# Kernel tuning notes

Hardware: AMD Instinct MI355X
Metric: run time of the kernel (lower is better)

## Reference

```python
import jax, jax.numpy as jnp
import numpy as np

N_NODES = 50000


def setup_inputs() -> dict:
    key = jax.random.key(0)
    k1, k2, k3, k4, k5 = jax.random.split(key, 5)
    N, E, D, U = N_NODES, 1600000, 128, 128
    node_features = jax.random.normal(k1, (N, D), dtype=jnp.float32)
    edge_src = jax.random.randint(k2, (E,), 0, N, dtype=jnp.int32)
    edge_dst = jax.random.randint(k3, (E,), 0, N, dtype=jnp.int32)
    edge_weight = jax.random.uniform(k4, (E,), dtype=jnp.float32)
    W = jax.random.normal(k5, (D, U), dtype=jnp.float32) * (1.0 / np.sqrt(D))
    b = jnp.zeros((U,), dtype=jnp.float32)
    return {"node_features": node_features, "edge_src": edge_src,
            "edge_dst": edge_dst, "edge_weight": edge_weight, "W": W, "b": b}


def reference(node_features, edge_src, edge_dst, edge_weight, W, b):
    # embedding_lookup_sparse_v2(..., combiner='mean'):
    #   agg[i] = sum_{e: src[e]=i} w[e] * feat[dst[e]] / sum_{e: src[e]=i} w[e]
    gathered = node_features[edge_dst] * edge_weight[:, None]        # [E, D]
    num = jax.ops.segment_sum(gathered, edge_src, num_segments=N_NODES)   # [N, D]
    den = jax.ops.segment_sum(edge_weight, edge_src, num_segments=N_NODES)  # [N]
    agg = num / jnp.maximum(den, 1e-12)[:, None]
    # Dense(units, activation='relu'); dropout is identity at inference
    return jax.nn.relu(agg @ W + b)
```

## Files before the change

kernel.cpp:

```cpp
#include <hip/hip_runtime.h>
#include <hip/hip_bf16.h>


typedef unsigned int vuint4 __attribute__((ext_vector_type(4)));
typedef short bf16x8 __attribute__((ext_vector_type(8)));
typedef float f32x4 __attribute__((ext_vector_type(4)));

#define SRCSH 8
#define BNODES 256
#define BCAP 9728
#define PCAP 11776
#define NBLK 512

__device__ __forceinline__ unsigned short f2bf(float f) {
    unsigned u = __float_as_uint(f);
    unsigned r = (u + 0x7fff + ((u >> 16) & 1)) >> 16;
    return (unsigned short)r;
}
__device__ __forceinline__ float bf2f(unsigned short h) {
    return __uint_as_float(((unsigned)h) << 16);
}

__global__ __launch_bounds__(256)
void histA_kernel(const float* __restrict__ feat, ushort* __restrict__ featb,
                  const float* __restrict__ W, ushort* __restrict__ WT,
                  const int* __restrict__ esrc, int* __restrict__ cnt,
                  int E, int nbuk, int N, int D) {
    __shared__ int hcnt[256];
    int tid = threadIdx.x, blk = blockIdx.x;

    {
        int gid = blk * 256 + tid;
        int gstr = NBLK * 256;
        int nf4 = N * D / 4;
        for (int i = gid; i < nf4; i += gstr) {
            float4 v = ((const float4*)feat)[i];
            ushort4 r;
            r.x = f2bf(v.x); r.y = f2bf(v.y); r.z = f2bf(v.z); r.w = f2bf(v.w);
            ((ushort4*)featb)[i] = r;
        }
        int nw = D * D;
        for (int i = gid; i < nw; i += gstr) {
            int u = i >> 7, k = i & 127;
            WT[i] = f2bf(W[k * 128 + u]);
        }
    }

    hcnt[tid] = 0;
    __syncthreads();

    int per = ((E + NBLK - 1) / NBLK + 3) & ~3;
    int lo = blk * per;
    int hi = lo + per; if (hi > E) hi = E;
    for (int i4 = (lo >> 2) + tid; i4 < (hi >> 2); i4 += 256) {
        int4 s = ((const int4*)esrc)[i4];
        atomicAdd(&hcnt[s.x >> SRCSH], 1);
        atomicAdd(&hcnt[s.y >> SRCSH], 1);
        atomicAdd(&hcnt[s.z >> SRCSH], 1);
        atomicAdd(&hcnt[s.w >> SRCSH], 1);
    }
    __syncthreads();
    if (tid < nbuk) cnt[blk * nbuk + tid] = hcnt[tid];
}

__global__ __launch_bounds__(256)
void scanB_kernel(const int* __restrict__ cnt, int* __restrict__ hbase,
                  int* __restrict__ gtot, int nbuk) {
    int lane = threadIdx.x & 63, wid = threadIdx.x >> 6;
    int b = blockIdx.x * 4 + wid;
    if (b >= nbuk) return;

    int v[8]; int run = 0;
    #pragma unroll
    for (int i = 0; i < 8; ++i) {
        v[i] = cnt[(lane * 8 + i) * nbuk + b];
        run += v[i];
    }
    int x = run;
    #pragma unroll
    for (int off = 1; off < 64; off <<= 1) {
        int y = __shfl_up(x, off, 64);
        if (lane >= off) x += y;
    }
    int excl = x - run;
    #pragma unroll
    for (int i = 0; i < 8; ++i) {
        hbase[b * NBLK + lane * 8 + i] = excl;
        excl += v[i];
    }
    if (lane == 63) gtot[b] = x;
}

__global__ __launch_bounds__(256)
void scatterC_kernel(const int* __restrict__ esrc, const int* __restrict__ edst,
                     const float* __restrict__ ew, const int* __restrict__ hbase,
                     unsigned long long* __restrict__ staging, int E, int nbuk) {
    __shared__ int hb[256];
    __shared__ int hoff[256];
    int tid = threadIdx.x, blk = blockIdx.x;
    if (tid < nbuk) { hb[tid] = hbase[tid * NBLK + blk]; }
    hoff[tid] = 0;
    __syncthreads();

    int per = ((E + NBLK - 1) / NBLK + 3) & ~3;
    int lo = blk * per;
    int hi = lo + per; if (hi > E) hi = E;
    for (int i4 = (lo >> 2) + tid; i4 < (hi >> 2); i4 += 256) {
        int4 s = ((const int4*)esrc)[i4];
        int4 d = ((const int4*)edst)[i4];
        float4 w = ((const float4*)ew)[i4];
        #pragma unroll
        for (int k = 0; k < 4; ++k) {
            int sv = (k == 0) ? s.x : (k == 1) ? s.y : (k == 2) ? s.z : s.w;
            int dv = (k == 0) ? d.x : (k == 1) ? d.y : (k == 2) ? d.z : d.w;
            float wv = (k == 0) ? w.x : (k == 1) ? w.y : (k == 2) ? w.z : w.w;
            int b = sv >> SRCSH;
            int pos = hb[b] + atomicAdd(&hoff[b], 1);
            if (pos < BCAP) {
                unsigned long long v = ((unsigned long long)__float_as_uint(wv) << 32)
                                     | ((unsigned long long)(sv & (BNODES - 1)) << 16)
                                     | (unsigned long long)(unsigned)dv;
                staging[(size_t)b * BCAP + pos] = v;
            }
        }
    }
}

__global__ __launch_bounds__(256)
void finB_kernel(const int* __restrict__ gtot, const unsigned long long* __restrict__ staging,
                 unsigned* __restrict__ pay4, int* __restrict__ rs, int* __restrict__ re, int N) {
    __shared__ int hist[BNODES];
    __shared__ int hcur[BNODES];
    __shared__ int ws[4];
    int b = blockIdx.x, tid = threadIdx.x;
    hist[tid] = 0;
    __syncthreads();

    int m = gtot[b]; if (m > BCAP) m = BCAP;
    size_t sbase = (size_t)b * BCAP;
    for (int i = tid; i < m; i += 256) {
        unsigned long long v = staging[sbase + i];
        atomicAdd(&hist[(int)((v >> 16) & (BNODES - 1))], 1);
    }
    __syncthreads();

    int lane = tid & 63, wid = tid >> 6;
    int h = hist[tid];
    int p = (h + 7) & ~7;
    int x = p;
    #pragma unroll
    for (int off = 1; off < 64; off <<= 1) {
        int y = __shfl_up(x, off, 64);
        if (lane >= off) x += y;
    }
    if (lane == 63) ws[wid] = x;
    __syncthreads();
    if (tid == 0) { int a = 0; for (int w = 0; w < 4; ++w) { int t = ws[w]; ws[w] = a; a += t; } }
    __syncthreads();
    int excl = ws[wid] + x - p;

    int gb = b * PCAP;
    hcur[tid] = excl;
    int n = b * BNODES + tid;
    if (n < N) { rs[n] = gb + excl; re[n] = gb + excl + p; }
    for (int i = excl + h; i < excl + p; ++i) pay4[gb + i] = 0;
    __syncthreads();

    for (int i = tid; i < m; i += 256) {
        unsigned long long v = staging[sbase + i];
        int s8 = (int)((v >> 16) & (BNODES - 1));
        int pos = atomicAdd(&hcur[s8], 1);
        unsigned wbf = f2bf(__uint_as_float((unsigned)(v >> 32)));
        pay4[gb + pos] = (wbf << 16) | (unsigned)(v & 0xffffu);
    }
}

__global__ __launch_bounds__(256, 8)
void agg_kernel(const ushort* __restrict__ featb, const unsigned* __restrict__ pay4,
                const int* __restrict__ rs, const int* __restrict__ re,
                ushort* __restrict__ aggb, int N) {
    int tid = threadIdx.x, lane = tid & 63, wid = tid >> 6;
    const ushort2* feat2 = (const ushort2*)featb;
    ushort2* agg2 = (ushort2*)aggb;

    int n0 = (blockIdx.x * 4 + wid) * 4;
    #pragma unroll
    for (int j = 0; j < 4; ++j) {
        int n = n0 + j;
        if (n >= N) break;
        int p = rs[n], pend = re[n];
        float ax = 0.f, ay = 0.f, ws = 0.f;
        for (; p < pend; p += 8) {
            vuint4 qa = __builtin_nontemporal_load((const vuint4*)(pay4 + p));
            vuint4 qb = __builtin_nontemporal_load((const vuint4*)(pay4 + p + 4));
            unsigned q[8] = {qa.x, qa.y, qa.z, qa.w, qb.x, qb.y, qb.z, qb.w};
            ushort2 f[8];
            #pragma unroll
            for (int k = 0; k < 8; ++k)
                f[k] = feat2[(q[k] & 0xffffu) * 64 + lane];
            #pragma unroll
            for (int k = 0; k < 8; ++k) {
                float w = bf2f((unsigned short)(q[k] >> 16));
                ax += w * bf2f(f[k].x);
                ay += w * bf2f(f[k].y);
                ws += w;
            }
        }
        float inv = 1.f / fmaxf(ws, 1e-12f);
        ushort2 o;
        o.x = f2bf(ax * inv);
        o.y = f2bf(ay * inv);
        agg2[(size_t)n * 64 + lane] = o;
    }
}

__global__ __launch_bounds__(256)
void gemm_kernel(const ushort* __restrict__ aggb, const ushort* __restrict__ WT,
                 const float* __restrict__ bias, float* __restrict__ out, int ntiles) {
    int tid = threadIdx.x, lane = tid & 63, wid = tid >> 6;
    int tile = blockIdx.x * 4 + wid;
    if (tile >= ntiles) return;
    int m = lane & 15, quad = lane >> 4;

    f32x4 acc[8];
    #pragma unroll
    for (int t = 0; t < 8; ++t) acc[t] = (f32x4){0.f, 0.f, 0.f, 0.f};

    #pragma unroll
    for (int ks = 0; ks < 4; ++ks) {
        bf16x8 a = *(const bf16x8*)(aggb + ((size_t)(tile * 16 + m) * 128 + ks * 32 + quad * 8));
        #pragma unroll
        for (int nt = 0; nt < 8; ++nt) {
            bf16x8 bfr = *(const bf16x8*)(WT + ((nt * 16 + m) * 128 + ks * 32 + quad * 8));
            acc[nt] = __builtin_amdgcn_mfma_f32_16x16x32_bf16(a, bfr, acc[nt], 0, 0, 0);
        }
    }

    #pragma unroll
    for (int nt = 0; nt < 8; ++nt) {
        int col = nt * 16 + m;
        float bv = bias[col];
        #pragma unroll
        for (int r = 0; r < 4; ++r) {
            int row = tile * 16 + quad * 4 + r;
            float v = fmaxf(acc[nt][r] + bv, 0.f);
            __builtin_nontemporal_store(v, out + (size_t)row * 128 + col);
        }
    }
}

extern "C" void kernel_launch(void* const* d_in, const int* in_sizes, int n_in,
                              void* d_out, int out_size, void* d_ws, size_t ws_size,
                              hipStream_t stream) {
    const float* feat = (const float*)d_in[0];
    const int*   esrc = (const int*)d_in[1];
    const int*   edst = (const int*)d_in[2];
    const float* ew   = (const float*)d_in[3];
    const float* W    = (const float*)d_in[4];
    const float* bias = (const float*)d_in[5];
    float* out = (float*)d_out;

    const int D = 128;
    int N = in_sizes[0] / D;
    int E = in_sizes[1];
    int nbuk = (N + BNODES - 1) >> SRCSH;

    unsigned long long* staging = (unsigned long long*)d_ws;
    int* cnt   = (int*)(staging + (size_t)nbuk * BCAP);
    int* hbase = cnt + (size_t)NBLK * nbuk;
    int* gtot  = hbase + (size_t)nbuk * NBLK;
    int* rs    = gtot + nbuk;
    int* re    = rs + N;
    unsigned* pay4 = (unsigned*)(re + N);
    ushort* featb = (ushort*)(pay4 + (size_t)nbuk * PCAP);
    ushort* aggb  = featb + (size_t)N * D;
    ushort* WT    = aggb + (size_t)N * D;

    histA_kernel<<<NBLK, 256, 0, stream>>>(feat, featb, W, WT, esrc, cnt, E, nbuk, N, D);
    scanB_kernel<<<(nbuk + 3) / 4, 256, 0, stream>>>(cnt, hbase, gtot, nbuk);
    scatterC_kernel<<<NBLK, 256, 0, stream>>>(esrc, edst, ew, hbase, staging, E, nbuk);
    finB_kernel<<<nbuk, 256, 0, stream>>>(gtot, staging, pay4, rs, re, N);
    agg_kernel<<<N / 16, 256, 0, stream>>>(featb, pay4, rs, re, aggb, N);
    int ntiles = N / 16;
    gemm_kernel<<<(ntiles + 3) / 4, 256, 0, stream>>>(aggb, WT, bias, out, ntiles);
}
```

Measured before the change: 227.0 us.

## Software-pipeline payload loads and use grid-stride node loop in aggregation kernel

The aggregation kernel now prefetches the next 8-edge payload chunk while the current chunk's feature gathers are processed, so payload load latency is hidden behind the gathers. The launch switches from one block per 16 nodes to a fixed grid of 2048 blocks, with each wave striding over nodes. The bf16 unpacking uses masks and shifts instead of conversion helpers, and the accumulation uses a 2-wide float vector that may map to packed FMA. The prefetch adds registers per thread, and the node order changes, which may alter load balance and cache locality.

```diff
diff --git a/kernel.cpp b/kernel.cpp
--- a/kernel.cpp
+++ b/kernel.cpp
@@ -5,12 +5,14 @@
 typedef unsigned int vuint4 __attribute__((ext_vector_type(4)));
 typedef short bf16x8 __attribute__((ext_vector_type(8)));
 typedef float f32x4 __attribute__((ext_vector_type(4)));
+typedef float f32x2 __attribute__((ext_vector_type(2)));
 
 #define SRCSH 8
 #define BNODES 256
 #define BCAP 9728
 #define PCAP 11776
 #define NBLK 512
+#define AGG_NBLK 2048
 
 __device__ __forceinline__ unsigned short f2bf(float f) {
     unsigned u = __float_as_uint(f);
@@ -183,33 +185,44 @@
     const ushort2* feat2 = (const ushort2*)featb;
     ushort2* agg2 = (ushort2*)aggb;
 
-    int n0 = (blockIdx.x * 4 + wid) * 4;
-    #pragma unroll
-    for (int j = 0; j < 4; ++j) {
-        int n = n0 + j;
-        if (n >= N) break;
+    const int NW = AGG_NBLK * 4;
+    for (int n = blockIdx.x * 4 + wid; n < N; n += NW) {
         int p = rs[n], pend = re[n];
-        float ax = 0.f, ay = 0.f, ws = 0.f;
-        for (; p < pend; p += 8) {
+        f32x2 axy = (f32x2){0.f, 0.f};
+        float wsum = 0.f;
+
+        if (p < pend) {
             vuint4 qa = __builtin_nontemporal_load((const vuint4*)(pay4 + p));
             vuint4 qb = __builtin_nontemporal_load((const vuint4*)(pay4 + p + 4));
-            unsigned q[8] = {qa.x, qa.y, qa.z, qa.w, qb.x, qb.y, qb.z, qb.w};
-            ushort2 f[8];
-            #pragma unroll
-            for (int k = 0; k < 8; ++k)
-                f[k] = feat2[(q[k] & 0xffffu) * 64 + lane];
-            #pragma unroll
-            for (int k = 0; k < 8; ++k) {
-                float w = bf2f((unsigned short)(q[k] >> 16));
-                ax += w * bf2f(f[k].x);
-                ay += w * bf2f(f[k].y);
-                ws += w;
+            while (p < pend) {
+                p += 8;
+                vuint4 na, nb;
+                bool more = p < pend;
+                if (more) {
+                    na = __builtin_nontemporal_load((const vuint4*)(pay4 + p));
+                    nb = __builtin_nontemporal_load((const vuint4*)(pay4 + p + 4));
+                }
+                unsigned q[8] = {qa.x, qa.y, qa.z, qa.w, qb.x, qb.y, qb.z, qb.w};
+                unsigned fu[8];
+                #pragma unroll
+                for (int k = 0; k < 8; ++k)
+                    fu[k] = *(const unsigned*)&feat2[(q[k] & 0xffffu) * 64 + lane];
+                #pragma unroll
+                for (int k = 0; k < 8; ++k) {
+                    float w = __uint_as_float(q[k] & 0xffff0000u);
+                    f32x2 f;
+                    f.x = __uint_as_float(fu[k] << 16);
+                    f.y = __uint_as_float(fu[k] & 0xffff0000u);
+                    axy += w * f;
+                    wsum += w;
+                }
+                qa = na; qb = nb;
             }
         }
-        float inv = 1.f / fmaxf(ws, 1e-12f);
+        float inv = 1.f / fmaxf(wsum, 1e-12f);
         ushort2 o;
-        o.x = f2bf(ax * inv);
-        o.y = f2bf(ay * inv);
+        o.x = f2bf(axy.x * inv);
+        o.y = f2bf(axy.y * inv);
         agg2[(size_t)n * 64 + lane] = o;
     }
 }
@@ -280,7 +293,7 @@
     scanB_kernel<<<(nbuk + 3) / 4, 256, 0, stream>>>(cnt, hbase, gtot, nbuk);
     scatterC_kernel<<<NBLK, 256, 0, stream>>>(esrc, edst, ew, hbase, staging, E, nbuk);
     finB_kernel<<<nbuk, 256, 0, stream>>>(gtot, staging, pay4, rs, re, N);
-    agg_kernel<<<N / 16, 256, 0, stream>>>(featb, pay4, rs, re, aggb, N);
+    agg_kernel<<<AGG_NBLK, 256, 0, stream>>>(featb, pay4, rs, re, aggb, N);
     int ntiles = N / 16;
     gemm_kernel<<<(ntiles + 3) / 4, 256, 0, stream>>>(aggb, WT, bias, out, ntiles);
 }
```

Result: no change. 226.5 us (-0.2%).
